# Performance work log

Hardware: AMD Instinct MI355X
Metric: run time of the kernel (lower is better)

Reference implementation:

```python
import jax, jax.numpy as jnp
import numpy as np

N = 30000      # nodes of type 'A'
IN = 128       # in_channels = hidden*2
H = 64         # hidden_channels
OUT = 64
M = 4          # number of metapaths (seq len for attention)
E = 480000     # edges per relation
NH = 8         # num_heads
HD = OUT // NH # head dim = 8
FF = 2048      # transformer dim_feedforward (torch default)
L = 2          # transformer layers
EPS = 1e-5


def setup_inputs() -> dict:
    key = jax.random.key(0)
    ks = iter(jax.random.split(key, 64))
    nk = lambda: next(ks)
    rn = lambda shape, s=0.05: (jax.random.normal(nk(), shape, jnp.float32) * s)
    x = jax.random.normal(nk(), (N, IN), jnp.float32)
    edge_index = jax.random.randint(nk(), (M, 2, E), 0, N, dtype=jnp.int32)
    counts = jnp.array([3.0, 1.0, 2.0, 2.0], jnp.float32)
    mp_weights = counts / counts.sum()
    inp = dict(x=x, edge_index=edge_index, mp_weights=mp_weights,
               W0=rn((M, H, IN)), b0=rn((M, H)), Wl=rn((M, H, IN)), bl=rn((M, H)),
               W1=rn((M, H, IN)), b1=rn((M, H)), Wo=rn((M, OUT, H)), bo=rn((M, OUT)),
               tinw=rn((L, 3 * OUT, OUT)), tinb=rn((L, 3 * OUT)),
               tow=rn((L, OUT, OUT)), tob=rn((L, OUT)),
               ln1g=jnp.ones((L, OUT)), ln1b=jnp.zeros((L, OUT)),
               ff1w=rn((L, FF, OUT)), ff1b=rn((L, FF)),
               ff2w=rn((L, OUT, FF)), ff2b=rn((L, OUT)),
               ln2g=jnp.ones((L, OUT)), ln2b=jnp.zeros((L, OUT)),
               r1w=rn((OUT, OUT)), r1b=rn((OUT,)), r2w=rn((1, OUT)), r2b=rn((1,)))
    return inp


def _layer_norm(v, g, b):
    mu = v.mean(-1, keepdims=True)
    var = ((v - mu) ** 2).mean(-1, keepdims=True)
    return (v - mu) / jnp.sqrt(var + EPS) * g + b


def reference(x, edge_index, mp_weights, W0, b0, Wl, bl, W1, b1, Wo, bo,
              tinw, tinb, tow, tob, ln1g, ln1b, ff1w, ff1b, ff2w, ff2b,
              ln2g, ln2b, r1w, r1b, r2w, r2b):
    n = x.shape[0]
    # ---- per-metapath GNN: gather + scatter-add + 3 fused linears ----
    embs = []
    for m in range(M):
        src, dst = edge_index[m, 0], edge_index[m, 1]
        # flow='target_to_source', aggr='add': agg[i] = sum_{e: src[e]==i} h[dst[e]]
        agg = jnp.zeros_like(x).at[src].add(x[dst])
        # w_l(agg) + w_0(h) + w_1(x), with h == x (forward passes x=h=h_dict[dst])
        h = jax.nn.relu(agg @ Wl[m].T + bl[m] + x @ (W0[m] + W1[m]).T + (b0[m] + b1[m]))
        embs.append(h @ Wo[m].T + bo[m])  # out_proj on updated start-type feats
    e = jnp.stack(embs, axis=1) * mp_weights[None, :, None]  # (N, M, OUT)

    # ---- 2-layer post-norm TransformerEncoder (batch_first, eval/no dropout) ----
    for l in range(L):
        qkv = e @ tinw[l].T + tinb[l]                       # (N, M, 3*OUT)
        q, k, v = jnp.split(qkv, 3, axis=-1)
        split = lambda t: t.reshape(n, M, NH, HD).transpose(0, 2, 1, 3)  # (N,NH,M,HD)
        q, k, v = split(q), split(k), split(v)
        attn = jax.nn.softmax(jnp.einsum('nhqd,nhkd->nhqk', q, k) / np.float32(np.sqrt(HD)), axis=-1)
        o = jnp.einsum('nhqk,nhkd->nhqd', attn, v).transpose(0, 2, 1, 3).reshape(n, M, OUT)
        o = o @ tow[l].T + tob[l]
        e = _layer_norm(e + o, ln1g[l], ln1b[l])
        f = jax.nn.relu(e @ ff1w[l].T + ff1b[l]) @ ff2w[l].T + ff2b[l]
        e = _layer_norm(e + f, ln2g[l], ln2b[l])

    pooled = e.mean(axis=1)                                  # (N, OUT)
    out = jax.nn.relu(pooled @ r1w.T + r1b) @ r2w.T + r2b    # (N, 1)
    return out[:, 0]
```

## Files before the change

### kernel.cpp

```cpp
#include <hip/hip_runtime.h>
#include <hip/hip_bf16.h>
#include <math.h>

#define N_NODES 30000
#define M_P     4
#define E_EDGES 480000
#define N_TOK   (N_NODES * 4)
#define N_ROWS  (M_P * N_NODES)
#define SLOTS   30
#define LN_EPS  1e-5f

typedef short bf16x8 __attribute__((ext_vector_type(8)));
typedef float f32x4  __attribute__((ext_vector_type(4)));
#define MFMA_B16(a, b, c) __builtin_amdgcn_mfma_f32_16x16x32_bf16(a, b, c, 0, 0, 0)

__device__ inline unsigned short f2bf(float f) {
    union { float f; unsigned u; } v; v.f = f;
    unsigned r = v.u + 0x7fffu + ((v.u >> 16) & 1u);
    return (unsigned short)(r >> 16);
}
__device__ inline unsigned pack2bf(float a, float b) {
    union { __hip_bfloat162 h; unsigned u; } cv;
    cv.h = __float22bfloat162_rn(make_float2(a, b));
    return cv.u;
}
__device__ inline float bf2f(short s) {
    union { unsigned u; float f; } v; v.u = ((unsigned)(unsigned short)s) << 16;
    return v.f;
}
__device__ inline bf16x8 mk_frag(const float4& a, const float4& b) {
    union { uint4 u; bf16x8 v; } cv;
    cv.u = make_uint4(pack2bf(a.x, a.y), pack2bf(a.z, a.w),
                      pack2bf(b.x, b.y), pack2bf(b.z, b.w));
    return cv.v;
}

__global__ __launch_bounds__(256, 2) void k_lin_yz(
    const float* __restrict__ x,
    const float* __restrict__ W0, const float* __restrict__ b0,
    const float* __restrict__ Wl, const float* __restrict__ bl,
    const float* __restrict__ W1, const float* __restrict__ b1,
    float* __restrict__ y, float* __restrict__ z)
{
    __shared__ float xT[128][68];
    __shared__ float wT[128][68];
    const int t     = threadIdx.x;
    const int m     = blockIdx.y >> 1;
    const int which = blockIdx.y & 1;
    const int node0 = blockIdx.x * 64;

    #pragma unroll
    for (int i = 0; i < 8; ++i) {
        const int node = (t & 31) + 32 * (i & 1);
        const int kq   = (t >> 5) + 8 * (i >> 1);
        float4 v = make_float4(0.f, 0.f, 0.f, 0.f);
        const int n = node0 + node;
        if (n < N_NODES) v = *(const float4*)(x + n * 128 + kq * 4);
        xT[kq * 4 + 0][node] = v.x; xT[kq * 4 + 1][node] = v.y;
        xT[kq * 4 + 2][node] = v.z; xT[kq * 4 + 3][node] = v.w;
    }
    #pragma unroll
    for (int i = 0; i < 8; ++i) {
        const int h  = (t & 31) + 32 * (i & 1);
        const int kq = (t >> 5) + 8 * (i >> 1);
        float4 v;
        if (which) {
            v = *(const float4*)(W0 + (m * 64 + h) * 128 + kq * 4);
            const float4 v2 = *(const float4*)(W1 + (m * 64 + h) * 128 + kq * 4);
            v.x += v2.x; v.y += v2.y; v.z += v2.z; v.w += v2.w;
        } else {
            v = *(const float4*)(Wl + (m * 64 + h) * 128 + kq * 4);
        }
        wT[kq * 4 + 0][h] = v.x; wT[kq * 4 + 1][h] = v.y;
        wT[kq * 4 + 2][h] = v.z; wT[kq * 4 + 3][h] = v.w;
    }
    __syncthreads();

    const int tx = t & 15, ty = t >> 4;
    const int hb = tx * 4, nb = ty * 4;
    float acc[4][4] = {};
    #pragma unroll 8
    for (int k = 0; k < 128; ++k) {
        const float4 a = *(const float4*)&xT[k][nb];
        const float4 b = *(const float4*)&wT[k][hb];
        acc[0][0] += a.x * b.x; acc[0][1] += a.x * b.y; acc[0][2] += a.x * b.z; acc[0][3] += a.x * b.w;
        acc[1][0] += a.y * b.x; acc[1][1] += a.y * b.y; acc[1][2] += a.y * b.z; acc[1][3] += a.y * b.w;
        acc[2][0] += a.z * b.x; acc[2][1] += a.z * b.y; acc[2][2] += a.z * b.z; acc[2][3] += a.z * b.w;
        acc[3][0] += a.w * b.x; acc[3][1] += a.w * b.y; acc[3][2] += a.w * b.z; acc[3][3] += a.w * b.w;
    }
    float bias[4] = {0.f, 0.f, 0.f, 0.f};
    if (which) {
        #pragma unroll
        for (int j = 0; j < 4; ++j)
            bias[j] = b0[m * 64 + hb + j] + b1[m * 64 + hb + j] + bl[m * 64 + hb + j];
    }
    float* outp = which ? z : y;
    #pragma unroll
    for (int i = 0; i < 4; ++i) {
        const int n = node0 + nb + i;
        if (n < N_NODES) {
            float4 v = make_float4(acc[i][0] + bias[0], acc[i][1] + bias[1],
                                   acc[i][2] + bias[2], acc[i][3] + bias[3]);
            *(float4*)(outp + (m * N_NODES + n) * 64 + hb) = v;
        }
    }
}

__global__ __launch_bounds__(256) void k_fill(
    const int* __restrict__ ei, unsigned short* __restrict__ bins,
    const float* __restrict__ y, float* __restrict__ aggh)
{
    const int base = blockIdx.x * 1024 + threadIdx.x;
    int rows[4], dsts[4];
    #pragma unroll
    for (int i = 0; i < 4; ++i) {
        const int g = base + i * 256;
        const int m = g / E_EDGES;
        const int e = g - m * E_EDGES;
        rows[i] = m * N_NODES + ei[(m * 2) * E_EDGES + e];
        dsts[i] = ei[(m * 2 + 1) * E_EDGES + e];
    }
    int pos[4];
    #pragma unroll
    for (int i = 0; i < 4; ++i)
        pos[i] = atomicAdd((int*)bins + rows[i] * 16, 1);
    #pragma unroll
    for (int i = 0; i < 4; ++i) {
        if (pos[i] < SLOTS) {
            bins[rows[i] * 32 + 2 + pos[i]] = (unsigned short)dsts[i];
        } else {
            const int m = rows[i] / N_NODES;
            const float* yr = y + ((size_t)m * N_NODES + dsts[i]) * 64;
            for (int f = 0; f < 64; ++f)
                unsafeAtomicAdd(&aggh[(size_t)rows[i] * 64 + f], yr[f]);
        }
    }
}

__global__ __launch_bounds__(256) void k_gather(
    const unsigned short* __restrict__ bins,
    const float* __restrict__ y, float* __restrict__ aggh)
{
    const int w = threadIdx.x >> 6, lane = threadIdx.x & 63;
    const int row = blockIdx.x * 4 + w;
    const int m = row / N_NODES;
    const float* ym = y + (size_t)m * N_NODES * 64;
    const int v = (lane < 32) ? bins[row * 32 + lane] : 0;
    const int v0 = __shfl(v, 0), v1 = __shfl(v, 1);
    const int tot = (v0 & 0xffff) | (v1 << 16);
    const int cnt = min(tot, SLOTS);
    float acc = (tot > SLOTS) ? aggh[(size_t)row * 64 + lane] : 0.f;
    for (int j = 0; j < cnt; ++j) {
        const int r = __shfl(v, j + 2);
        acc += ym[r * 64 + lane];
    }
    aggh[(size_t)row * 64 + lane] = acc;
}

__global__ __launch_bounds__(256) void k_emb(
    const float* __restrict__ aggh, const float* __restrict__ z,
    const float* __restrict__ Wo, const float* __restrict__ bo,
    const float* __restrict__ mpw, float* __restrict__ e)
{
    __shared__ float hT[64][20];
    __shared__ float WoT[64][64];
    const int t = threadIdx.x;
    const int node0 = blockIdx.x * 16;

    for (int m = 0; m < 4; ++m) {
        #pragma unroll
        for (int i = 0; i < 4; ++i) {
            const int o  = (t & 15) + 16 * i;
            const int kq = t >> 4;
            const float4 v = *(const float4*)(Wo + (m * 64 + o) * 64 + kq * 4);
            WoT[kq * 4 + 0][o] = v.x; WoT[kq * 4 + 1][o] = v.y;
            WoT[kq * 4 + 2][o] = v.z; WoT[kq * 4 + 3][o] = v.w;
        }
        {
            const int node = t & 15, kq = t >> 4;
            const int n = node0 + node;
            const float4 a = *(const float4*)(aggh + (m * N_NODES + n) * 64 + kq * 4);
            const float4 b = *(const float4*)(z + (m * N_NODES + n) * 64 + kq * 4);
            hT[kq * 4 + 0][node] = fmaxf(a.x + b.x, 0.f);
            hT[kq * 4 + 1][node] = fmaxf(a.y + b.y, 0.f);
            hT[kq * 4 + 2][node] = fmaxf(a.z + b.z, 0.f);
            hT[kq * 4 + 3][node] = fmaxf(a.w + b.w, 0.f);
        }
        __syncthreads();
        const int o = t & 63, nl4 = (t >> 6) * 4;
        float acc[4] = {};
        #pragma unroll 8
        for (int k = 0; k < 64; ++k) {
            const float bw = WoT[k][o];
            const float4 a = *(const float4*)&hT[k][nl4];
            acc[0] += a.x * bw; acc[1] += a.y * bw; acc[2] += a.z * bw; acc[3] += a.w * bw;
        }
        const float bb = bo[m * 64 + o];
        const float w  = mpw[m];
        #pragma unroll
        for (int i = 0; i < 4; ++i)
            e[((node0 + nl4 + i) * 4 + m) * 64 + o] = (acc[i] + bb) * w;
        __syncthreads();
    }
}

__global__ __launch_bounds__(256, 3) void k_attn_mfma(
    const float* __restrict__ e,
    const unsigned short* __restrict__ wqkv_s, const float* __restrict__ tinb,
    const unsigned short* __restrict__ tow_s, const float* __restrict__ tob,
    const float* __restrict__ ln1g, const float* __restrict__ ln1b,
    float* __restrict__ eout, int l)
{
    __shared__ __align__(16) short QK[17408];
    __shared__ __align__(16) short Vb[9216];
    const int t = threadIdx.x;
    const int w = t >> 6, lane = t & 63;
    const int m_ = lane & 15, qc = lane >> 4;
    const int tok0 = blockIdx.x * 128;
    short* QKw = &QK[w * 4352];
    short* Vw  = &Vb[w * 2304];

    bf16x8 xb[2][2];
    #pragma unroll
    for (int nt = 0; nt < 2; ++nt)
        #pragma unroll
        for (int h = 0; h < 2; ++h) {
            const int tok = tok0 + w * 32 + nt * 16 + m_;
            const int k0 = h * 32 + qc * 8;
            float4 a = make_float4(0.f, 0.f, 0.f, 0.f), b = a;
            if (tok < N_TOK) {
                a = *(const float4*)(e + tok * 64 + k0);
                b = *(const float4*)(e + tok * 64 + k0 + 4);
            }
            xb[nt][h] = mk_frag(a, b);
        }

    const unsigned short* Wq = wqkv_s + l * 12288;
    f32x4 acc[12][2];
    #pragma unroll
    for (int ft = 0; ft < 12; ++ft) {
        const bf16x8 wa0 = *(const bf16x8*)(Wq + (ft * 2 + 0) * 512 + lane * 8);
        const bf16x8 wa1 = *(const bf16x8*)(Wq + (ft * 2 + 1) * 512 + lane * 8);
        const float4 bv = *(const float4*)(tinb + l * 192 + ft * 16 + qc * 4);
        f32x4 c0; c0[0] = bv.x; c0[1] = bv.y; c0[2] = bv.z; c0[3] = bv.w;
        f32x4 c1 = c0;
        c0 = MFMA_B16(wa0, xb[0][0], c0); c0 = MFMA_B16(wa1, xb[0][1], c0);
        c1 = MFMA_B16(wa0, xb[1][0], c1); c1 = MFMA_B16(wa1, xb[1][1], c1);
        acc[ft][0] = c0; acc[ft][1] = c1;
    }
    #pragma unroll
    for (int ft = 0; ft < 8; ++ft)
        #pragma unroll
        for (int nt = 0; nt < 2; ++nt) {
            const int addr = (nt * 16 + m_) * 136 + ft * 16 + qc * 4;
            *(uint2*)&QKw[addr] = make_uint2(pack2bf(acc[ft][nt][0], acc[ft][nt][1]),
                                             pack2bf(acc[ft][nt][2], acc[ft][nt][3]));
        }
    #pragma unroll
    for (int ft = 8; ft < 12; ++ft)
        #pragma unroll
        for (int nt = 0; nt < 2; ++nt) {
            const int addr = (nt * 16 + m_) * 72 + (ft - 8) * 16 + qc * 4;
            *(uint2*)&Vw[addr] = make_uint2(pack2bf(acc[ft][nt][0], acc[ft][nt][1]),
                                            pack2bf(acc[ft][nt][2], acc[ft][nt][3]));
        }

    {
        const int node = lane >> 3, head = lane & 7;
        float kk[4][8], vv[4][8], qv[4][8];
        #pragma unroll
        for (int j2 = 0; j2 < 4; ++j2) {
            const bf16x8 kr = *(const bf16x8*)&QKw[(node * 4 + j2) * 136 + 64 + head * 8];
            const bf16x8 vr = *(const bf16x8*)&Vw[(node * 4 + j2) * 72 + head * 8];
            const bf16x8 qr = *(const bf16x8*)&QKw[(node * 4 + j2) * 136 + head * 8];
            #pragma unroll
            for (int d = 0; d < 8; ++d) {
                kk[j2][d] = bf2f(kr[d]); vv[j2][d] = bf2f(vr[d]); qv[j2][d] = bf2f(qr[d]);
            }
        }
        const float scale = 0.35355339059327373f;
        const int nt2 = node >> 2, hq = head >> 2, qq = head & 3;
        #pragma unroll
        for (int i = 0; i < 4; ++i) {
            float s[4];
            #pragma unroll
            for (int j2 = 0; j2 < 4; ++j2) {
                float a2 = 0.f;
                #pragma unroll
                for (int d = 0; d < 8; ++d) a2 += qv[i][d] * kk[j2][d];
                s[j2] = a2 * scale;
            }
            const float mx = fmaxf(fmaxf(s[0], s[1]), fmaxf(s[2], s[3]));
            float p[4], sum = 0.f;
            #pragma unroll
            for (int j2 = 0; j2 < 4; ++j2) { p[j2] = __expf(s[j2] - mx); sum += p[j2]; }
            const float inv = 1.f / sum;
            float o[8];
            #pragma unroll
            for (int d = 0; d < 8; ++d)
                o[d] = (p[0] * vv[0][d] + p[1] * vv[1][d] + p[2] * vv[2][d] + p[3] * vv[3][d]) * inv;
            const int n = (node & 3) * 4 + i;
            *(uint4*)&QKw[(nt2 * 2 + hq) * 512 + qq * 128 + n * 8] =
                make_uint4(pack2bf(o[0], o[1]), pack2bf(o[2], o[3]),
                           pack2bf(o[4], o[5]), pack2bf(o[6], o[7]));
        }
    }

    bf16x8 ob[2][2];
    #pragma unroll
    for (int nt = 0; nt < 2; ++nt)
        #pragma unroll
        for (int h = 0; h < 2; ++h)
            ob[nt][h] = *(const bf16x8*)&QKw[(nt * 2 + h) * 512 + lane * 8];
    const unsigned short* Tw = tow_s + l * 4096;
    f32x4 acc2[4][2] = {};
    #pragma unroll
    for (int ot = 0; ot < 4; ++ot) {
        const bf16x8 t0 = *(const bf16x8*)(Tw + (ot * 2 + 0) * 512 + lane * 8);
        const bf16x8 t1 = *(const bf16x8*)(Tw + (ot * 2 + 1) * 512 + lane * 8);
        acc2[ot][0] = MFMA_B16(t0, ob[0][0], acc2[ot][0]);
        acc2[ot][0] = MFMA_B16(t1, ob[0][1], acc2[ot][0]);
        acc2[ot][1] = MFMA_B16(t0, ob[1][0], acc2[ot][1]);
        acc2[ot][1] = MFMA_B16(t1, ob[1][1], acc2[ot][1]);
    }

    float4 tbv[4], gv[4], bv2[4];
    #pragma unroll
    for (int ot = 0; ot < 4; ++ot) {
        const int o = l * 64 + ot * 16 + qc * 4;
        tbv[ot] = *(const float4*)(tob + o);
        gv[ot]  = *(const float4*)(ln1g + o);
        bv2[ot] = *(const float4*)(ln1b + o);
    }
    #pragma unroll
    for (int nt = 0; nt < 2; ++nt) {
        const int tok = tok0 + w * 32 + nt * 16 + m_;
        const bool valid = tok < N_TOK;
        float v[4][4];
        float s = 0.f;
        #pragma unroll
        for (int ot = 0; ot < 4; ++ot) {
            float4 rs = make_float4(0.f, 0.f, 0.f, 0.f);
            if (valid) rs = *(const float4*)(e + tok * 64 + ot * 16 + qc * 4);
            v[ot][0] = acc2[ot][nt][0] + tbv[ot].x + rs.x;
            v[ot][1] = acc2[ot][nt][1] + tbv[ot].y + rs.y;
            v[ot][2] = acc2[ot][nt][2] + tbv[ot].z + rs.z;
            v[ot][3] = acc2[ot][nt][3] + tbv[ot].w + rs.w;
            s += v[ot][0] + v[ot][1] + v[ot][2] + v[ot][3];
        }
        s += __shfl_xor(s, 16); s += __shfl_xor(s, 32);
        const float mean = s * (1.f / 64.f);
        float vs = 0.f;
        #pragma unroll
        for (int ot = 0; ot < 4; ++ot)
            #pragma unroll
            for (int r = 0; r < 4; ++r) { v[ot][r] -= mean; vs += v[ot][r] * v[ot][r]; }
        vs += __shfl_xor(vs, 16); vs += __shfl_xor(vs, 32);
        const float rr = rsqrtf(vs * (1.f / 64.f) + LN_EPS);
        if (valid) {
            #pragma unroll
            for (int ot = 0; ot < 4; ++ot) {
                float4 o4 = make_float4(v[ot][0] * rr * gv[ot].x + bv2[ot].x,
                                        v[ot][1] * rr * gv[ot].y + bv2[ot].y,
                                        v[ot][2] * rr * gv[ot].z + bv2[ot].z,
                                        v[ot][3] * rr * gv[ot].w + bv2[ot].w);
                *(float4*)(eout + tok * 64 + ot * 16 + qc * 4) = o4;
            }
        }
    }
}

__global__ __launch_bounds__(256) void k_wshuf(
    const float* __restrict__ ff1w, const float* __restrict__ ff2w,
    const float* __restrict__ tinw, const float* __restrict__ tow,
    unsigned short* __restrict__ w1s, unsigned short* __restrict__ w2s,
    unsigned short* __restrict__ wqkv_s, unsigned short* __restrict__ tow_s)
{
    const int g = blockIdx.x * 256 + threadIdx.x;
    {
        const int l = g >> 17, r2 = g & 131071;
        const int f = r2 >> 6, k = r2 & 63;
        const int c = f >> 6, fc = f & 63, ft = fc >> 4, m = fc & 15;
        const int h = k >> 5, q = (k >> 3) & 3, j = k & 7;
        w1s[l * 131072 + c * 4096 + (ft * 2 + h) * 512 + (q * 16 + m) * 8 + j] = f2bf(ff1w[g]);
    }
    {
        const int l = g >> 17, r2 = g & 131071;
        const int o = r2 >> 11, f = r2 & 2047;
        const int c = f >> 6, fc = f & 63, h = fc >> 5, q = (fc >> 3) & 3, j = fc & 7;
        const int ot = o >> 4, m = o & 15;
        w2s[l * 131072 + c * 4096 + (ot * 2 + h) * 512 + (q * 16 + m) * 8 + j] = f2bf(ff2w[g]);
    }
    if (g < 2 * 192 * 64) {
        const int l = g / 12288, r2 = g - l * 12288;
        const int f = r2 >> 6, k = r2 & 63;
        const int ft = f >> 4, m = f & 15;
        const int h = k >> 5, q = (k >> 3) & 3, j = k & 7;
        wqkv_s[l * 12288 + (ft * 2 + h) * 512 + (q * 16 + m) * 8 + j] = f2bf(tinw[g]);
    }
    if (g < 2 * 64 * 64) {
        const int l = g >> 12, r2 = g & 4095;
        const int o = r2 >> 6, k = r2 & 63;
        const int ot = o >> 4, m = o & 15;
        const int h = k >> 5, q = (k >> 3) & 3, j = k & 7;
        tow_s[l * 4096 + (ot * 2 + h) * 512 + (q * 16 + m) * 8 + j] = f2bf(tow[g]);
    }
}

__global__ __launch_bounds__(256, 4) void k_ffn_mfma(
    const float* __restrict__ e,
    const unsigned short* __restrict__ w1s, const unsigned short* __restrict__ w2s,
    const float* __restrict__ ff1b, const float* __restrict__ ff2b,
    const float* __restrict__ ln2g, const float* __restrict__ ln2b,
    float* __restrict__ eout, int l)
{
    __shared__ __align__(16) short Act[8192];
    __shared__ __align__(16) short Wb[8192];
    const int t = threadIdx.x;
    const int w = t >> 6, lane = t & 63;
    const int m_ = lane & 15, qc = lane >> 4;
    const int tok0 = blockIdx.x * 128;
    short* Aw = &Act[w * 2048];

    bf16x8 xb[2][2];
    #pragma unroll
    for (int nt = 0; nt < 2; ++nt)
        #pragma unroll
        for (int h = 0; h < 2; ++h) {
            const int tok = tok0 + w * 32 + nt * 16 + m_;
            const int k0 = h * 32 + qc * 8;
            float4 a = make_float4(0.f, 0.f, 0.f, 0.f), b = a;
            if (tok < N_TOK) {
                a = *(const float4*)(e + tok * 64 + k0);
                b = *(const float4*)(e + tok * 64 + k0 + 4);
            }
            xb[nt][h] = mk_frag(a, b);
        }

    const uint4* gw1 = (const uint4*)(w1s + l * 131072);
    const uint4* gw2 = (const uint4*)(w2s + l * 131072);
    uint4 p0 = gw1[t], p1 = gw1[t + 256], p2 = gw2[t], p3 = gw2[t + 256];
    *(uint4*)&Wb[t * 8] = p0;            *(uint4*)&Wb[(t + 256) * 8] = p1;
    *(uint4*)&Wb[4096 + t * 8] = p2;     *(uint4*)&Wb[4096 + (t + 256) * 8] = p3;

    f32x4 acc[4][2] = {};

    for (int c = 0; c < 32; ++c) {
        __syncthreads();
        if (c < 31) {
            p0 = gw1[(c + 1) * 512 + t];       p1 = gw1[(c + 1) * 512 + t + 256];
            p2 = gw2[(c + 1) * 512 + t];       p3 = gw2[(c + 1) * 512 + t + 256];
        }
        #pragma unroll
        for (int ft = 0; ft < 4; ++ft) {
            const bf16x8 wa0 = *(const bf16x8*)&Wb[(ft * 2 + 0) * 512 + lane * 8];
            const bf16x8 wa1 = *(const bf16x8*)&Wb[(ft * 2 + 1) * 512 + lane * 8];
            const float4 bv = *(const float4*)(ff1b + l * 2048 + c * 64 + ft * 16 + qc * 4);
            f32x4 c0; c0[0] = bv.x; c0[1] = bv.y; c0[2] = bv.z; c0[3] = bv.w;
            f32x4 c1 = c0;
            c0 = MFMA_B16(wa0, xb[0][0], c0); c0 = MFMA_B16(wa1, xb[0][1], c0);
            c1 = MFMA_B16(wa0, xb[1][0], c1); c1 = MFMA_B16(wa1, xb[1][1], c1);
            const int ha = ft >> 1, qa = (ft & 1) * 2 + (qc >> 1), jo = (qc & 1) * 4;
            const int boff = ha * 512 + qa * 128 + m_ * 8 + jo;
            *(uint2*)&Aw[boff] =
                make_uint2(pack2bf(fmaxf(c0[0], 0.f), fmaxf(c0[1], 0.f)),
                           pack2bf(fmaxf(c0[2], 0.f), fmaxf(c0[3], 0.f)));
            *(uint2*)&Aw[boff + 1024] =
                make_uint2(pack2bf(fmaxf(c1[0], 0.f), fmaxf(c1[1], 0.f)),
                           pack2bf(fmaxf(c1[2], 0.f), fmaxf(c1[3], 0.f)));
        }
        bf16x8 ab[2][2];
        #pragma unroll
        for (int nt = 0; nt < 2; ++nt)
            #pragma unroll
            for (int h = 0; h < 2; ++h)
                ab[nt][h] = *(const bf16x8*)&Aw[(nt * 2 + h) * 512 + lane * 8];
        #pragma unroll
        for (int ot = 0; ot < 4; ++ot) {
            const bf16x8 w20 = *(const bf16x8*)&Wb[4096 + (ot * 2 + 0) * 512 + lane * 8];
            const bf16x8 w21 = *(const bf16x8*)&Wb[4096 + (ot * 2 + 1) * 512 + lane * 8];
            acc[ot][0] = MFMA_B16(w20, ab[0][0], acc[ot][0]);
            acc[ot][0] = MFMA_B16(w21, ab[0][1], acc[ot][0]);
            acc[ot][1] = MFMA_B16(w20, ab[1][0], acc[ot][1]);
            acc[ot][1] = MFMA_B16(w21, ab[1][1], acc[ot][1]);
        }
        __syncthreads();
        if (c < 31) {
            *(uint4*)&Wb[t * 8] = p0;            *(uint4*)&Wb[(t + 256) * 8] = p1;
            *(uint4*)&Wb[4096 + t * 8] = p2;     *(uint4*)&Wb[4096 + (t + 256) * 8] = p3;
        }
    }

    float4 fb2v[4], gv[4], bv2[4];
    #pragma unroll
    for (int ot = 0; ot < 4; ++ot) {
        const int o = l * 64 + ot * 16 + qc * 4;
        fb2v[ot] = *(const float4*)(ff2b + o);
        gv[ot]   = *(const float4*)(ln2g + o);
        bv2[ot]  = *(const float4*)(ln2b + o);
    }
    #pragma unroll
    for (int nt = 0; nt < 2; ++nt) {
        const int tok = tok0 + w * 32 + nt * 16 + m_;
        const bool valid = tok < N_TOK;
        float v[4][4];
        float s = 0.f;
        #pragma unroll
        for (int ot = 0; ot < 4; ++ot) {
            float4 rs = make_float4(0.f, 0.f, 0.f, 0.f);
            if (valid) rs = *(const float4*)(e + tok * 64 + ot * 16 + qc * 4);
            v[ot][0] = acc[ot][nt][0] + fb2v[ot].x + rs.x;
            v[ot][1] = acc[ot][nt][1] + fb2v[ot].y + rs.y;
            v[ot][2] = acc[ot][nt][2] + fb2v[ot].z + rs.z;
            v[ot][3] = acc[ot][nt][3] + fb2v[ot].w + rs.w;
            s += v[ot][0] + v[ot][1] + v[ot][2] + v[ot][3];
        }
        s += __shfl_xor(s, 16); s += __shfl_xor(s, 32);
        const float mean = s * (1.f / 64.f);
        float vs = 0.f;
        #pragma unroll
        for (int ot = 0; ot < 4; ++ot)
            #pragma unroll
            for (int r = 0; r < 4; ++r) { v[ot][r] -= mean; vs += v[ot][r] * v[ot][r]; }
        vs += __shfl_xor(vs, 16); vs += __shfl_xor(vs, 32);
        const float rr = rsqrtf(vs * (1.f / 64.f) + LN_EPS);
        if (valid) {
            #pragma unroll
            for (int ot = 0; ot < 4; ++ot) {
                float4 o4 = make_float4(v[ot][0] * rr * gv[ot].x + bv2[ot].x,
                                        v[ot][1] * rr * gv[ot].y + bv2[ot].y,
                                        v[ot][2] * rr * gv[ot].z + bv2[ot].z,
                                        v[ot][3] * rr * gv[ot].w + bv2[ot].w);
                *(float4*)(eout + tok * 64 + ot * 16 + qc * 4) = o4;
            }
        }
    }
}

__global__ __launch_bounds__(256) void k_reg(
    const float* __restrict__ e,
    const float* __restrict__ r1w, const float* __restrict__ r1b,
    const float* __restrict__ r2w, const float* __restrict__ r2b,
    float* __restrict__ out)
{
    __shared__ float r1T[64][64];
    __shared__ float pld[4][64];
    const int t = threadIdx.x;
    #pragma unroll
    for (int i = 0; i < 4; ++i) {
        const int j  = (t & 15) + 16 * i;
        const int kq = t >> 4;
        const float4 v = *(const float4*)(r1w + j * 64 + kq * 4);
        r1T[kq * 4 + 0][j] = v.x; r1T[kq * 4 + 1][j] = v.y;
        r1T[kq * 4 + 2][j] = v.z; r1T[kq * 4 + 3][j] = v.w;
    }
    const int w = t >> 6, lane = t & 63;
    const int n = blockIdx.x * 4 + w;
    const float p = 0.25f * (e[(n * 4 + 0) * 64 + lane] + e[(n * 4 + 1) * 64 + lane] +
                             e[(n * 4 + 2) * 64 + lane] + e[(n * 4 + 3) * 64 + lane]);
    pld[w][lane] = p;
    __syncthreads();
    float acc = r1b[lane];
    #pragma unroll 8
    for (int k = 0; k < 64; ++k) acc += pld[w][k] * r1T[k][lane];
    acc = fmaxf(acc, 0.f);
    float partial = acc * r2w[lane];
    partial += __shfl_xor(partial, 1);  partial += __shfl_xor(partial, 2);
    partial += __shfl_xor(partial, 4);  partial += __shfl_xor(partial, 8);
    partial += __shfl_xor(partial, 16); partial += __shfl_xor(partial, 32);
    if (lane == 0) out[n] = partial + r2b[0];
}

extern "C" void kernel_launch(void* const* d_in, const int* in_sizes, int n_in,
                              void* d_out, int out_size, void* d_ws, size_t ws_size,
                              hipStream_t stream) {
    const float* x    = (const float*)d_in[0];
    const int*   ei   = (const int*)d_in[1];
    const float* mpw  = (const float*)d_in[2];
    const float* W0   = (const float*)d_in[3];
    const float* b0   = (const float*)d_in[4];
    const float* Wl   = (const float*)d_in[5];
    const float* bl   = (const float*)d_in[6];
    const float* W1   = (const float*)d_in[7];
    const float* b1   = (const float*)d_in[8];
    const float* Wo   = (const float*)d_in[9];
    const float* bo   = (const float*)d_in[10];
    const float* tinw = (const float*)d_in[11];
    const float* tinb = (const float*)d_in[12];
    const float* tow  = (const float*)d_in[13];
    const float* tob  = (const float*)d_in[14];
    const float* ln1g = (const float*)d_in[15];
    const float* ln1b = (const float*)d_in[16];
    const float* ff1w = (const float*)d_in[17];
    const float* ff1b = (const float*)d_in[18];
    const float* ff2w = (const float*)d_in[19];
    const float* ff2b = (const float*)d_in[20];
    const float* ln2g = (const float*)d_in[21];
    const float* ln2b = (const float*)d_in[22];
    const float* r1w  = (const float*)d_in[23];
    const float* r1b  = (const float*)d_in[24];
    const float* r2w  = (const float*)d_in[25];
    const float* r2b  = (const float*)d_in[26];

    const size_t CH = (size_t)M_P * N_NODES * 64;
    float* y    = (float*)d_ws;
    float* zz   = y + CH;
    float* aggh = zz + CH;
    float* e    = aggh + CH;
    unsigned short* w1s    = (unsigned short*)y;
    unsigned short* w2s    = w1s + 262144;
    unsigned short* wqkv_s = w2s + 262144;
    unsigned short* tow_s  = wqkv_s + 24576;
    unsigned short* bins = (unsigned short*)e;

    hipMemsetAsync(bins, 0, (size_t)N_ROWS * 64, stream);
    hipMemsetAsync(aggh, 0, CH * sizeof(float), stream);
    k_lin_yz<<<dim3(469, 8), 256, 0, stream>>>(x, W0, b0, Wl, bl, W1, b1, y, zz);
    k_fill<<<(M_P * E_EDGES) / 1024, 256, 0, stream>>>(ei, bins, y, aggh);
    k_gather<<<N_ROWS / 4, 256, 0, stream>>>(bins, y, aggh);
    k_emb<<<N_NODES / 16, 256, 0, stream>>>(aggh, zz, Wo, bo, mpw, e);
    k_wshuf<<<1024, 256, 0, stream>>>(ff1w, ff2w, tinw, tow, w1s, w2s, wqkv_s, tow_s);
    for (int l = 0; l < 2; ++l) {
        k_attn_mfma<<<(N_TOK + 127) / 128, 256, 0, stream>>>(e, wqkv_s, tinb, tow_s, tob,
                                                             ln1g, ln1b, e, l);
        k_ffn_mfma<<<(N_TOK + 127) / 128, 256, 0, stream>>>(e, w1s, w2s, ff1b, ff2b,
                                                            ln2g, ln2b, e, l);
    }
    k_reg<<<N_NODES / 4, 256, 0, stream>>>(e, r1w, r1b, r2w, r2b, (float*)d_out);
}
```

Measured before the change: 693.5 us.

## Move GNN input linears to bf16 MFMA with pre-shuffled weights; unroll gather

Replaces the fp32 LDS-tiled GEMM that produced y and z with a bf16 MFMA kernel. A new kernel converts Wl and W0+W1 into a fragment-ordered bf16 layout, and x is packed into bf16 fragments directly from global memory. Separately, the gather loop now keeps four independent accumulators to expose more memory-level parallelism. This trades fp32 precision in the node linears for bf16, adds a small weight-shuffle launch, and places the shuffled weights in scratch space inside the e buffer.

```diff
diff --git a/kernel.cpp b/kernel.cpp
--- a/kernel.cpp
+++ b/kernel.cpp
@@ -35,74 +35,73 @@
     return cv.v;
 }
 
-__global__ __launch_bounds__(256, 2) void k_lin_yz(
-    const float* __restrict__ x,
-    const float* __restrict__ W0, const float* __restrict__ b0,
-    const float* __restrict__ Wl, const float* __restrict__ bl,
-    const float* __restrict__ W1, const float* __restrict__ b1,
+__global__ __launch_bounds__(256) void k_wshuf_gnn(
+    const float* __restrict__ Wl, const float* __restrict__ W0, const float* __restrict__ W1,
+    unsigned short* __restrict__ wgnn)
+{
+    const int g = blockIdx.x * 256 + threadIdx.x;
+    const int which = g >> 15;
+    const int r = g & 32767;
+    const int m = r >> 13;
+    const int r2 = r & 8191;
+    const int row = r2 >> 7, k = r2 & 127;
+    const int ot = row >> 4, mm = row & 15;
+    const int hh = k >> 5, q = (k >> 3) & 3, j = k & 7;
+    float v;
+    if (which == 0) v = Wl[(m * 64 + row) * 128 + k];
+    else            v = W0[(m * 64 + row) * 128 + k] + W1[(m * 64 + row) * 128 + k];
+    wgnn[((which * 4 + m) * 16 + ot * 4 + hh) * 512 + (q * 16 + mm) * 8 + j] = f2bf(v);
+}
+
+__global__ __launch_bounds__(256) void k_lin_mfma(
+    const float* __restrict__ x, const unsigned short* __restrict__ wgnn,
+    const float* __restrict__ b0, const float* __restrict__ bl, const float* __restrict__ b1,
     float* __restrict__ y, float* __restrict__ z)
 {
-    __shared__ float xT[128][68];
-    __shared__ float wT[128][68];
-    const int t     = threadIdx.x;
-    const int m     = blockIdx.y >> 1;
-    const int which = blockIdx.y & 1;
-    const int node0 = blockIdx.x * 64;
-
-    #pragma unroll
-    for (int i = 0; i < 8; ++i) {
-        const int node = (t & 31) + 32 * (i & 1);
-        const int kq   = (t >> 5) + 8 * (i >> 1);
-        float4 v = make_float4(0.f, 0.f, 0.f, 0.f);
-        const int n = node0 + node;
-        if (n < N_NODES) v = *(const float4*)(x + n * 128 + kq * 4);
-        xT[kq * 4 + 0][node] = v.x; xT[kq * 4 + 1][node] = v.y;
-        xT[kq * 4 + 2][node] = v.z; xT[kq * 4 + 3][node] = v.w;
-    }
-    #pragma unroll
-    for (int i = 0; i < 8; ++i) {
-        const int h  = (t & 31) + 32 * (i & 1);
-        const int kq = (t >> 5) + 8 * (i >> 1);
-        float4 v;
+    const int t = threadIdx.x;
+    const int w = t >> 6, lane = t & 63;
+    const int m_ = lane & 15, qc = lane >> 4;
+    const int mw = blockIdx.y;
+    const int which = mw >> 2, m = mw & 3;
+    const int node = blockIdx.x * 64 + w * 16 + m_;
+
+    bf16x8 xb[4];
+    #pragma unroll
+    for (int hh = 0; hh < 4; ++hh) {
+        float4 a = make_float4(0.f, 0.f, 0.f, 0.f), b = a;
+        if (node < N_NODES) {
+            a = *(const float4*)(x + node * 128 + hh * 32 + qc * 8);
+            b = *(const float4*)(x + node * 128 + hh * 32 + qc * 8 + 4);
+        }
+        xb[hh] = mk_frag(a, b);
+    }
+
+    const unsigned short* Wg = wgnn + mw * 16 * 512;
+    f32x4 acc[4];
+    #pragma unroll
+    for (int ot = 0; ot < 4; ++ot) {
+        f32x4 c = {};
         if (which) {
-            v = *(const float4*)(W0 + (m * 64 + h) * 128 + kq * 4);
-            const float4 v2 = *(const float4*)(W1 + (m * 64 + h) * 128 + kq * 4);
-            v.x += v2.x; v.y += v2.y; v.z += v2.z; v.w += v2.w;
-        } else {
-            v = *(const float4*)(Wl + (m * 64 + h) * 128 + kq * 4);
-        }
-        wT[kq * 4 + 0][h] = v.x; wT[kq * 4 + 1][h] = v.y;
-        wT[kq * 4 + 2][h] = v.z; wT[kq * 4 + 3][h] = v.w;
-    }
-    __syncthreads();
-
-    const int tx = t & 15, ty = t >> 4;
-    const int hb = tx * 4, nb = ty * 4;
-    float acc[4][4] = {};
-    #pragma unroll 8
-    for (int k = 0; k < 128; ++k) {
-        const float4 a = *(const float4*)&xT[k][nb];
-        const float4 b = *(const float4*)&wT[k][hb];
-        acc[0][0] += a.x * b.x; acc[0][1] += a.x * b.y; acc[0][2] += a.x * b.z; acc[0][3] += a.x * b.w;
-        acc[1][0] += a.y * b.x; acc[1][1] += a.y * b.y; acc[1][2] += a.y * b.z; acc[1][3] += a.y * b.w;
-        acc[2][0] += a.z * b.x; acc[2][1] += a.z * b.y; acc[2][2] += a.z * b.z; acc[2][3] += a.z * b.w;
-        acc[3][0] += a.w * b.x; acc[3][1] += a.w * b.y; acc[3][2] += a.w * b.z; acc[3][3] += a.w * b.w;
-    }
-    float bias[4] = {0.f, 0.f, 0.f, 0.f};
-    if (which) {
-        #pragma unroll
-        for (int j = 0; j < 4; ++j)
-            bias[j] = b0[m * 64 + hb + j] + b1[m * 64 + hb + j] + bl[m * 64 + hb + j];
+            const int o = m * 64 + ot * 16 + qc * 4;
+            const float4 v0 = *(const float4*)(b0 + o);
+            const float4 v1 = *(const float4*)(b1 + o);
+            const float4 vl = *(const float4*)(bl + o);
+            c[0] = v0.x + v1.x + vl.x; c[1] = v0.y + v1.y + vl.y;
+            c[2] = v0.z + v1.z + vl.z; c[3] = v0.w + v1.w + vl.w;
+        }
+        #pragma unroll
+        for (int hh = 0; hh < 4; ++hh) {
+            const bf16x8 wa = *(const bf16x8*)(Wg + (ot * 4 + hh) * 512 + lane * 8);
+            c = MFMA_B16(wa, xb[hh], c);
+        }
+        acc[ot] = c;
     }
     float* outp = which ? z : y;
-    #pragma unroll
-    for (int i = 0; i < 4; ++i) {
-        const int n = node0 + nb + i;
-        if (n < N_NODES) {
-            float4 v = make_float4(acc[i][0] + bias[0], acc[i][1] + bias[1],
-                                   acc[i][2] + bias[2], acc[i][3] + bias[3]);
-            *(float4*)(outp + (m * N_NODES + n) * 64 + hb) = v;
-        }
+    if (node < N_NODES) {
+        #pragma unroll
+        for (int ot = 0; ot < 4; ++ot)
+            *(float4*)(outp + ((size_t)m * N_NODES + node) * 64 + ot * 16 + qc * 4) =
+                *(float4*)&acc[ot];
     }
 }
 
@@ -149,12 +148,20 @@
     const int v0 = __shfl(v, 0), v1 = __shfl(v, 1);
     const int tot = (v0 & 0xffff) | (v1 << 16);
     const int cnt = min(tot, SLOTS);
-    float acc = (tot > SLOTS) ? aggh[(size_t)row * 64 + lane] : 0.f;
-    for (int j = 0; j < cnt; ++j) {
+    float a0 = (tot > SLOTS) ? aggh[(size_t)row * 64 + lane] : 0.f;
+    float a1 = 0.f, a2 = 0.f, a3 = 0.f;
+    int j = 0;
+    for (; j + 4 <= cnt; j += 4) {
+        const int r0 = __shfl(v, j + 2), r1 = __shfl(v, j + 3);
+        const int r2 = __shfl(v, j + 4), r3 = __shfl(v, j + 5);
+        a0 += ym[r0 * 64 + lane]; a1 += ym[r1 * 64 + lane];
+        a2 += ym[r2 * 64 + lane]; a3 += ym[r3 * 64 + lane];
+    }
+    for (; j < cnt; ++j) {
         const int r = __shfl(v, j + 2);
-        acc += ym[r * 64 + lane];
-    }
-    aggh[(size_t)row * 64 + lane] = acc;
+        a0 += ym[r * 64 + lane];
+    }
+    aggh[(size_t)row * 64 + lane] = (a0 + a1) + (a2 + a3);
 }
 
 __global__ __launch_bounds__(256) void k_emb(
@@ -612,10 +619,12 @@
     unsigned short* wqkv_s = w2s + 262144;
     unsigned short* tow_s  = wqkv_s + 24576;
     unsigned short* bins = (unsigned short*)e;
+    unsigned short* wgnn = (unsigned short*)((char*)e + 8 * 1024 * 1024);
 
     hipMemsetAsync(bins, 0, (size_t)N_ROWS * 64, stream);
     hipMemsetAsync(aggh, 0, CH * sizeof(float), stream);
-    k_lin_yz<<<dim3(469, 8), 256, 0, stream>>>(x, W0, b0, Wl, bl, W1, b1, y, zz);
+    k_wshuf_gnn<<<256, 256, 0, stream>>>(Wl, W0, W1, wgnn);
+    k_lin_mfma<<<dim3(469, 8), 256, 0, stream>>>(x, wgnn, b0, bl, b1, y, zz);
     k_fill<<<(M_P * E_EDGES) / 1024, 256, 0, stream>>>(ei, bins, y, aggh);
     k_gather<<<N_ROWS / 4, 256, 0, stream>>>(bins, y, aggh);
     k_emb<<<N_NODES / 16, 256, 0, stream>>>(aggh, zz, Wo, bo, mpw, e);
```

After: 596.6 us. 14.0% less time.
